# Kernel optimization log

Measured on AMD Instinct MI355X. Metric: run time of the kernel, lower is better.

Reference implementation:

```python
import jax, jax.numpy as jnp
import numpy as np

DIM = 2048
NUM_HEADS = 16
HEAD_DIM = DIM // NUM_HEADS
HIDDEN = 4 * DIM
EPS = 1e-6


def rmsnorm(x, w):
    # Faithful to source: weight * (x * dim**-0.5 / sqrt(mean(x^2) + eps))
    scale = DIM ** -0.5
    norm = jnp.sqrt(jnp.mean(x * x, axis=-1, keepdims=True) + EPS)
    return w * (x * scale / norm)


def setup_inputs() -> dict:
    key = jax.random.key(0)
    ks = jax.random.split(key, 10)
    def init(k, shape, fan_in):
        return jax.random.normal(k, shape, dtype=jnp.float32) * (fan_in ** -0.5)
    return {
        "x": jax.random.normal(ks[0], (2, 2048, DIM), dtype=jnp.float32),
        "norm1_w": jnp.ones((DIM,), dtype=jnp.float32),
        "wq": init(ks[1], (DIM, DIM), DIM),
        "wk": init(ks[2], (HEAD_DIM, DIM), DIM),
        "wv": init(ks[3], (HEAD_DIM, DIM), DIM),
        "wo": init(ks[4], (DIM, DIM), DIM),
        "norm2_w": jnp.ones((DIM,), dtype=jnp.float32),
        "w1": init(ks[5], (HIDDEN, DIM), DIM),
        "w2": init(ks[6], (DIM, HIDDEN), HIDDEN),
        "w3": init(ks[7], (HIDDEN, DIM), DIM),
    }


def reference(x, norm1_w, wq, wk, wv, wo, norm2_w, w1, w2, w3):
    B, S, _ = x.shape
    # --- Multi-Query Attention (pre-norm) ---
    h = rmsnorm(x, norm1_w)
    q = h @ wq.T                                  # [B,S,D]
    k = h @ wk.T                                  # [B,S,hd] (shared across heads)
    v = h @ wv.T                                  # [B,S,hd]
    q = q.reshape(B, S, NUM_HEADS, HEAD_DIM)
    # scores: q @ k^T / sqrt(hd); k is broadcast (repeated) across heads
    scores = jnp.einsum('bshd,btd->bhst', q, k) / (HEAD_DIM ** 0.5)  # [B,H,S,S]
    probs = jax.nn.softmax(scores, axis=-1)
    attn = jnp.einsum('bhst,btd->bshd', probs, v).reshape(B, S, DIM)
    x = x + attn @ wo.T
    # --- SwiGLU FFN (pre-norm) ---
    h = rmsnorm(x, norm2_w)
    ffn = (jax.nn.silu(h @ w1.T) * (h @ w3.T)) @ w2.T
    return x + ffn
```

## Files before the change

kernel.cpp:

```cpp
#include <hip/hip_runtime.h>
#include <hip/hip_bf16.h>

typedef __attribute__((ext_vector_type(4))) float f32x4;
typedef __attribute__((ext_vector_type(8))) short s16x8;
typedef __attribute__((ext_vector_type(4))) short s16x4;
typedef __attribute__((ext_vector_type(2))) short s16x2;

#define MFMA_BF16 __builtin_amdgcn_mfma_f32_16x16x32_bf16

__device__ inline short f2bf(float f) {
  unsigned u = __float_as_uint(f);
  u = (u + 0x7FFFu + ((u >> 16) & 1u)) >> 16;
  return (short)u;
}
__device__ inline float bf2f(short s) {
  return __uint_as_float(((unsigned)(unsigned short)s) << 16);
}

#define DPPF(x, ctrl) __int_as_float(__builtin_amdgcn_update_dpp( \
    __float_as_int(x), __float_as_int(x), ctrl, 0xF, 0xF, false))
__device__ inline float rowmax16(float x) {
  x = fmaxf(x, DPPF(x, 0xB1));
  x = fmaxf(x, DPPF(x, 0x4E));
  x = fmaxf(x, DPPF(x, 0x124));
  x = fmaxf(x, DPPF(x, 0x128));
  return x;
}
__device__ inline float rowsum16(float x) {
  x += DPPF(x, 0xB1);
  x += DPPF(x, 0x4E);
  x += DPPF(x, 0x124);
  x += DPPF(x, 0x128);
  return x;
}

__global__ __launch_bounds__(256) void cvt_kernel(
    const float* __restrict__ in, short* __restrict__ out, int n, float scale)
{
  int idx = (blockIdx.x * 256 + threadIdx.x) * 8;
  if (idx >= n) return;
  f32x4 a = *(const f32x4*)(in + idx);
  f32x4 b = *(const f32x4*)(in + idx + 4);
  s16x8 o;
  #pragma unroll
  for (int j = 0; j < 4; ++j) { o[j] = f2bf(a[j] * scale); o[4 + j] = f2bf(b[j] * scale); }
  *(s16x8*)(out + idx) = o;
}

__global__ __launch_bounds__(256) void rmsnorm_kernel(
    const float* __restrict__ x, const float* __restrict__ w, short* __restrict__ out)
{
  size_t row = blockIdx.x;
  const float* xr = x + row * 2048;
  int base = threadIdx.x * 8;
  f32x4 a = *(const f32x4*)(xr + base);
  f32x4 b = *(const f32x4*)(xr + base + 4);
  float ss = a[0]*a[0] + a[1]*a[1] + a[2]*a[2] + a[3]*a[3]
           + b[0]*b[0] + b[1]*b[1] + b[2]*b[2] + b[3]*b[3];
  #pragma unroll
  for (int off = 1; off < 64; off <<= 1) ss += __shfl_xor(ss, off, 64);
  __shared__ float red[4];
  if ((threadIdx.x & 63) == 0) red[threadIdx.x >> 6] = ss;
  __syncthreads();
  float tot = red[0] + red[1] + red[2] + red[3];
  float rn = rsqrtf(tot * (1.0f / 2048.0f) + 1e-6f) * 0.022097086912079608f;
  f32x4 wa = *(const f32x4*)(w + base);
  f32x4 wb = *(const f32x4*)(w + base + 4);
  s16x8 o;
  #pragma unroll
  for (int j = 0; j < 4; ++j) {
    o[j]     = f2bf(a[j] * wa[j] * rn);
    o[4 + j] = f2bf(b[j] * wb[j] * rn);
  }
  *(s16x8*)(out + row * 2048 + base) = o;
}

template <int MODE>
__global__ __launch_bounds__(256, 2) void gemm_bt_kernel(
    const short* __restrict__ A, const short* __restrict__ B,
    void* __restrict__ Cv, const float* __restrict__ resid,
    int M, int N, int K)
{
  __shared__ short As[128 * 32];
  __shared__ short Bs[128 * 32];
  int tid = threadIdx.x;
  int lane = tid & 63;
  int w = tid >> 6;
  int r = lane & 15, g = lane >> 4;
  int wr = w >> 1, wc = w & 1;
  size_t row0 = (size_t)blockIdx.y * 128;
  size_t col0 = (size_t)blockIdx.x * 128;

  f32x4 acc[4][4];
  #pragma unroll
  for (int i = 0; i < 4; ++i)
    #pragma unroll
    for (int j = 0; j < 4; ++j) acc[i][j] = (f32x4){0.f, 0.f, 0.f, 0.f};

  const short* Ablk = A + row0 * K;
  const short* Bblk = B + col0 * K;
  int arow = tid >> 2;
  int akk = (tid & 3) << 3;

  for (int k0 = 0; k0 < K; k0 += 32) {
    #pragma unroll
    for (int i = 0; i < 2; ++i) {
      int chunk = i * 256 + tid;
      int rr = i * 64 + arow;
      __builtin_amdgcn_global_load_lds(
          (const __attribute__((address_space(1))) unsigned int*)(Ablk + (size_t)rr * K + k0 + akk),
          (__attribute__((address_space(3))) unsigned int*)(&As[chunk * 8]), 16, 0, 0);
      __builtin_amdgcn_global_load_lds(
          (const __attribute__((address_space(1))) unsigned int*)(Bblk + (size_t)rr * K + k0 + akk),
          (__attribute__((address_space(3))) unsigned int*)(&Bs[chunk * 8]), 16, 0, 0);
    }
    __syncthreads();
    s16x8 af[4], bfr[4];
    #pragma unroll
    for (int mm = 0; mm < 4; ++mm)
      af[mm] = *(const s16x8*)(&As[(wr * 64 + mm * 16 + r) * 32 + g * 8]);
    #pragma unroll
    for (int nn = 0; nn < 4; ++nn)
      bfr[nn] = *(const s16x8*)(&Bs[(wc * 64 + nn * 16 + r) * 32 + g * 8]);
    #pragma unroll
    for (int mm = 0; mm < 4; ++mm)
      #pragma unroll
      for (int nn = 0; nn < 4; ++nn)
        acc[mm][nn] = MFMA_BF16(af[mm], bfr[nn], acc[mm][nn], 0, 0, 0);
    __syncthreads();
  }

  #pragma unroll
  for (int mm = 0; mm < 4; ++mm) {
    #pragma unroll
    for (int nn = 0; nn < 4; ++nn) {
      #pragma unroll
      for (int j = 0; j < 4; ++j) {
        size_t rr = row0 + wr * 64 + mm * 16 + g * 4 + j;
        size_t cc = col0 + wc * 64 + nn * 16 + r;
        size_t idx = rr * (size_t)N + cc;
        if constexpr (MODE == 0) {
          ((short*)Cv)[idx] = f2bf(acc[mm][nn][j]);
        } else if constexpr (MODE == 1) {
          ((float*)Cv)[idx] = acc[mm][nn][j] + resid[idx];
        } else {
          short* gp = (short*)Cv;
          float gv = bf2f(gp[idx]);
          float sg = gv / (1.0f + __expf(-gv));
          gp[idx] = f2bf(sg * acc[mm][nn][j]);
        }
      }
    }
  }
}


#define STAGEA1(T)                                                             \
  _Pragma("unroll")                                                            \
  for (int i = 0; i < 4; ++i) {                                                \
    int lc = i * 256 + tid;                                                    \
    int rw = lc >> 3, ch = lc & 7;                                             \
    __builtin_amdgcn_global_load_lds(                                          \
        (const __attribute__((address_space(1))) unsigned int*)                \
            (Ablk + (size_t)rw * K + (T) * 64 + ((ch ^ (rw & 7)) << 3)),       \
        (__attribute__((address_space(3))) unsigned int*)                      \
            (&As[(T) & 1][lc * 8]), 16, 0, 0);                                 \
  }

#define STAGEB1(T)                                                             \
  _Pragma("unroll")                                                            \
  for (int i = 0; i < 4; ++i) {                                                \
    int lc = i * 256 + tid;                                                    \
    int rw = lc >> 3, ch = lc & 7;                                             \
    __builtin_amdgcn_global_load_lds(                                          \
        (const __attribute__((address_space(1))) unsigned int*)                \
            (Bblk + (size_t)rw * K + (T) * 64 + ((ch ^ (rw & 7)) << 3)),       \
        (__attribute__((address_space(3))) unsigned int*)                      \
            (&Bs[(T) & 1][lc * 8]), 16, 0, 0);                                 \
  }

#define LDK(KS, D)                                                             \
  _Pragma("unroll")                                                            \
  for (int mi = 0; mi < 4; ++mi) {                                             \
    int rowa = wr * 64 + mi * 16 + r;                                          \
    aR[mi] = *(const s16x8*)(&As[D][rowa * 64 + (((KS) * 4 + g) ^ (rowa & 7)) * 8]); \
  }                                                                            \
  _Pragma("unroll")                                                            \
  for (int ni = 0; ni < 4; ++ni) {                                             \
    int rowb = wc * 64 + ni * 16 + r;                                          \
    bR[ni] = *(const s16x8*)(&Bs[D][rowb * 64 + (((KS) * 4 + g) ^ (rowb & 7)) * 8]); \
  }

#define MF16A                                                                  \
  __builtin_amdgcn_s_setprio(1);                                               \
  _Pragma("unroll")                                                            \
  for (int mi = 0; mi < 4; ++mi)                                               \
    _Pragma("unroll")                                                          \
    for (int ni = 0; ni < 4; ++ni)                                             \
      acc[mi][ni] = MFMA_BF16(aR[mi], bR[ni], acc[mi][ni], 0, 0, 0);           \
  __builtin_amdgcn_s_setprio(0);

#define BAR __builtin_amdgcn_s_barrier()

template <int MODE>
__global__ __launch_bounds__(256, 2) void gemm128_kernel(
    const short* __restrict__ A, const short* __restrict__ B,
    void* __restrict__ Cv, const float* __restrict__ resid,
    int M, int N, int K)
{
  __shared__ short As[2][128 * 64];
  __shared__ short Bs[2][128 * 64];

  int tid = threadIdx.x;
  int lane = tid & 63;
  int w = tid >> 6;
  int r = lane & 15, g = lane >> 4;
  int wr = w >> 1, wc = w & 1;

  int nwg = gridDim.x * gridDim.y;
  int orig = blockIdx.y * gridDim.x + blockIdx.x;
  int swz = (orig & 7) * (nwg >> 3) + (orig >> 3);
  int bx = swz % gridDim.x, by = swz / gridDim.x;
  size_t row0 = (size_t)by * 128;
  size_t col0 = (size_t)bx * 128;

  const short* Ablk = A + row0 * K;
  const short* Bblk = B + col0 * K;

  f32x4 acc[4][4];
  #pragma unroll
  for (int i = 0; i < 4; ++i)
    #pragma unroll
    for (int j = 0; j < 4; ++j) acc[i][j] = (f32x4){0.f, 0.f, 0.f, 0.f};

  s16x8 aR[4], bR[4];
  int NT = K >> 6;

  STAGEA1(0); STAGEB1(0);

  for (int t = 0; t < NT; ++t) {
    int d = t & 1;
    bool nl = (t < NT - 1);
    if (nl) {
      STAGEA1(t + 1); STAGEB1(t + 1);
      asm volatile("s_waitcnt vmcnt(8)" ::: "memory");
    } else {
      asm volatile("s_waitcnt vmcnt(0)" ::: "memory");
    }
    BAR;
    LDK(0, d);
    MF16A;
    LDK(1, d);
    MF16A;
    BAR;
  }

  #pragma unroll
  for (int mi = 0; mi < 4; ++mi) {
    #pragma unroll
    for (int ni = 0; ni < 4; ++ni) {
      #pragma unroll
      for (int j = 0; j < 4; ++j) {
        size_t rr = row0 + wr * 64 + mi * 16 + g * 4 + j;
        size_t cc = col0 + wc * 64 + ni * 16 + r;
        size_t idx = rr * (size_t)N + cc;
        if constexpr (MODE == 0) {
          ((short*)Cv)[idx] = f2bf(acc[mi][ni][j]);
        } else if constexpr (MODE == 1) {
          ((float*)Cv)[idx] = acc[mi][ni][j] + resid[idx];
        } else {
          short* gp = (short*)Cv;
          float gv = bf2f(gp[idx]);
          float sg = gv / (1.0f + __expf(-gv));
          gp[idx] = f2bf(sg * acc[mi][ni][j]);
        }
      }
    }
  }
}

__global__ __launch_bounds__(256) void transpose_v_kernel(
    const short* __restrict__ kv, short* __restrict__ vt)
{
  __shared__ short t[64][65];
  int b = blockIdx.z;
  int s0 = blockIdx.x * 64;
  int d0 = blockIdx.y * 64;
  int tid = threadIdx.x;
  #pragma unroll
  for (int i = 0; i < 16; ++i) {
    int e = i * 256 + tid;
    int sr = e >> 6, dc = e & 63;
    t[sr][dc] = kv[(size_t)(b * 2048 + s0 + sr) * 256 + 128 + d0 + dc];
  }
  __syncthreads();
  #pragma unroll
  for (int i = 0; i < 16; ++i) {
    int e = i * 256 + tid;
    int dr = e >> 6, sc = e & 63;
    vt[(size_t)b * 128 * 2048 + (size_t)(d0 + dr) * 2048 + s0 + sc] = t[sc][dr];
  }
}

__global__ __launch_bounds__(256, 2) void attn_kernel(
    const short* __restrict__ q, const short* __restrict__ kv,
    const short* __restrict__ vt, short* __restrict__ out)
{
  const int S = 2048;
  int tid = threadIdx.x;
  int w = tid >> 6;
  int lane = tid & 63;
  int r = lane & 15, g = lane >> 4;
  int h = blockIdx.y, b = blockIdx.z;
  int qrow0 = blockIdx.x * 128 + w * 32;

  __shared__ short Ks[2][4096];
  __shared__ short Vs[2][4096];
  __shared__ short Ps[4][32][40];

  const short* kvsrc = kv + (size_t)b * S * 256;
  const short* vsrc  = vt + (size_t)b * 128 * S;

  const short* qbase = q + ((size_t)(b * S + qrow0 + r)) * 2048 + h * 128;
  s16x8 qa[2][4];
  #pragma unroll
  for (int gq = 0; gq < 2; ++gq)
    #pragma unroll
    for (int dc = 0; dc < 4; ++dc)
      qa[gq][dc] = *(const s16x8*)(qbase + gq * 16 * 2048 + dc * 32 + g * 8);

  f32x4 o[2][8];
  #pragma unroll
  for (int gq = 0; gq < 2; ++gq)
    #pragma unroll
    for (int dt = 0; dt < 8; ++dt) o[gq][dt] = (f32x4){0.f, 0.f, 0.f, 0.f};
  float m[2][4], l[2][4];
  #pragma unroll
  for (int gq = 0; gq < 2; ++gq)
    #pragma unroll
    for (int j = 0; j < 4; ++j) { m[gq][j] = -1e30f; l[gq][j] = 0.f; }

#define STAGE(KVT, BSEL)                                                        \
  {                                                                             \
    int kv0s = (KVT) * 32;                                                      \
    _Pragma("unroll")                                                           \
    for (int i = 0; i < 2; ++i) {                                               \
      int c = w * 64 + lane + i * 256;                                          \
      int krow = c >> 4, kcp = c & 15;                                          \
      __builtin_amdgcn_global_load_lds(                                         \
          (const __attribute__((address_space(1))) unsigned int*)               \
              (kvsrc + (size_t)(kv0s + krow) * 256 + ((kcp ^ (krow & 7)) << 3)),\
          (__attribute__((address_space(3))) unsigned int*)(&Ks[BSEL][c * 8]),  \
          16, 0, 0);                                                            \
      int vrow = c >> 2, vcp = c & 3;                                           \
      __builtin_amdgcn_global_load_lds(                                         \
          (const __attribute__((address_space(1))) unsigned int*)               \
              (vsrc + (size_t)vrow * S + kv0s + ((vcp ^ (vrow & 3)) << 3)),     \
          (__attribute__((address_space(3))) unsigned int*)(&Vs[BSEL][c * 8]),  \
          16, 0, 0);                                                            \
    }                                                                           \
  }

  STAGE(0, 0);
  __syncthreads();

  for (int it = 0; it < 64; ++it) {
    int cur = it & 1;
    if (it < 63) STAGE(it + 1, cur ^ 1);

    s16x8 kc0[4], kc1[4], vb[8];
    #pragma unroll
    for (int dc = 0; dc < 4; ++dc) {
      kc0[dc] = *(const s16x8*)(&Ks[cur][r * 128 + (((dc * 4 + g) ^ (r & 7)) << 3)]);
      kc1[dc] = *(const s16x8*)(&Ks[cur][(16 + r) * 128 + (((dc * 4 + g) ^ (r & 7)) << 3)]);
    }
    #pragma unroll
    for (int dt = 0; dt < 8; ++dt)
      vb[dt] = *(const s16x8*)(&Vs[cur][(dt * 16 + r) * 32 + ((g ^ (r & 3)) << 3)]);

    f32x4 sc0[2], sc1[2];
    #pragma unroll
    for (int gq = 0; gq < 2; ++gq) { sc0[gq] = (f32x4){0.f,0.f,0.f,0.f}; sc1[gq] = (f32x4){0.f,0.f,0.f,0.f}; }
    __builtin_amdgcn_s_setprio(1);
    #pragma unroll
    for (int dc = 0; dc < 4; ++dc) {
      #pragma unroll
      for (int gq = 0; gq < 2; ++gq) {
        sc0[gq] = MFMA_BF16(qa[gq][dc], kc0[dc], sc0[gq], 0, 0, 0);
        sc1[gq] = MFMA_BF16(qa[gq][dc], kc1[dc], sc1[gq], 0, 0, 0);
      }
    }
    __builtin_amdgcn_s_setprio(0);

    float p0[2][4], p1[2][4];
    #pragma unroll
    for (int gq = 0; gq < 2; ++gq) {
      float mx[4];
      #pragma unroll
      for (int j = 0; j < 4; ++j) mx[j] = rowmax16(fmaxf(sc0[gq][j], sc1[gq][j]));
      bool nd = (mx[0] > m[gq][0] + 8.f) | (mx[1] > m[gq][1] + 8.f)
              | (mx[2] > m[gq][2] + 8.f) | (mx[3] > m[gq][3] + 8.f);
      if (__any(nd)) {
        #pragma unroll
        for (int j = 0; j < 4; ++j) {
          float mn = fmaxf(m[gq][j], mx[j]);
          float alpha = __expf(m[gq][j] - mn);
          m[gq][j] = mn;
          l[gq][j] *= alpha;
          #pragma unroll
          for (int dt = 0; dt < 8; ++dt) o[gq][dt][j] *= alpha;
        }
      }
      #pragma unroll
      for (int j = 0; j < 4; ++j) {
        p0[gq][j] = __expf(sc0[gq][j] - m[gq][j]);
        p1[gq][j] = __expf(sc1[gq][j] - m[gq][j]);
        l[gq][j] += p0[gq][j] + p1[gq][j];
      }
      #pragma unroll
      for (int j = 0; j < 4; ++j) {
        Ps[w][gq * 16 + g * 4 + j][r]      = f2bf(p0[gq][j]);
        Ps[w][gq * 16 + g * 4 + j][16 + r] = f2bf(p1[gq][j]);
      }
    }
    asm volatile("s_waitcnt lgkmcnt(0)" ::: "memory");
    __builtin_amdgcn_sched_barrier(0);
    s16x8 pa0 = *(const s16x8*)(&Ps[w][r][g * 8]);
    s16x8 pa1 = *(const s16x8*)(&Ps[w][16 + r][g * 8]);
    __builtin_amdgcn_s_setprio(1);
    #pragma unroll
    for (int dt = 0; dt < 8; ++dt) {
      o[0][dt] = MFMA_BF16(pa0, vb[dt], o[0][dt], 0, 0, 0);
      o[1][dt] = MFMA_BF16(pa1, vb[dt], o[1][dt], 0, 0, 0);
    }
    __builtin_amdgcn_s_setprio(0);
    __syncthreads();
  }

  #pragma unroll
  for (int gq = 0; gq < 2; ++gq) {
    float linv[4];
    #pragma unroll
    for (int j = 0; j < 4; ++j) linv[j] = 1.0f / rowsum16(l[gq][j]);
    short* ob = out + ((size_t)(b * S + qrow0 + gq * 16)) * 2048 + h * 128;
    #pragma unroll
    for (int dt = 0; dt < 8; ++dt)
      #pragma unroll
      for (int j = 0; j < 4; ++j)
        ob[(size_t)(g * 4 + j) * 2048 + dt * 16 + r] = f2bf(o[gq][dt][j] * linv[j]);
  }
#undef STAGE
}

extern "C" void kernel_launch(void* const* d_in, const int* in_sizes, int n_in,
                              void* d_out, int out_size, void* d_ws, size_t ws_size,
                              hipStream_t stream) {
  const float* x   = (const float*)d_in[0];
  const float* n1w = (const float*)d_in[1];
  const float* wq  = (const float*)d_in[2];
  const float* wk  = (const float*)d_in[3];
  const float* wv  = (const float*)d_in[4];
  const float* wo  = (const float*)d_in[5];
  const float* n2w = (const float*)d_in[6];
  const float* w1  = (const float*)d_in[7];
  const float* w2  = (const float*)d_in[8];
  const float* w3  = (const float*)d_in[9];
  float* out = (float*)d_out;
  char* ws = (char*)d_ws;
  const size_t MB = 1ull << 20;
  short* wqb  = (short*)(ws);
  short* wob  = (short*)(ws + 8 * MB);
  short* w1b  = (short*)(ws + 16 * MB);
  short* w2b  = (short*)(ws + 48 * MB);
  short* w3b  = (short*)(ws + 80 * MB);
  short* wkvb = (short*)(ws + 112 * MB);
  short* h1   = (short*)(ws + 113 * MB);
  short* gbuf = (short*)(ws + 129 * MB);
  short* qb   = (short*)(ws + 129 * MB);
  short* kvb  = (short*)(ws + 145 * MB);
  short* vtb  = (short*)(ws + 147 * MB);

  const float qscale = 0.08838834764831845f;
  cvt_kernel<<<2048, 256, 0, stream>>>(wq, wqb, 4194304, qscale);
  cvt_kernel<<<128,  256, 0, stream>>>(wk, wkvb, 262144, 1.0f);
  cvt_kernel<<<128,  256, 0, stream>>>(wv, wkvb + 262144, 262144, 1.0f);
  cvt_kernel<<<2048, 256, 0, stream>>>(wo, wob, 4194304, 1.0f);
  cvt_kernel<<<8192, 256, 0, stream>>>(w1, w1b, 16777216, 1.0f);
  cvt_kernel<<<8192, 256, 0, stream>>>(w2, w2b, 16777216, 1.0f);
  cvt_kernel<<<8192, 256, 0, stream>>>(w3, w3b, 16777216, 1.0f);

  rmsnorm_kernel<<<4096, 256, 0, stream>>>(x, n1w, h1);
  gemm128_kernel<0><<<dim3(16, 32), 256, 0, stream>>>(h1, wqb, qb, nullptr, 4096, 2048, 2048);
  gemm_bt_kernel<0><<<dim3(2, 32), 256, 0, stream>>>(h1, wkvb, kvb, nullptr, 4096, 256, 2048);
  transpose_v_kernel<<<dim3(32, 2, 2), 256, 0, stream>>>(kvb, vtb);
  attn_kernel<<<dim3(16, 16, 2), 256, 0, stream>>>(qb, kvb, vtb, h1);
  gemm128_kernel<1><<<dim3(16, 32), 256, 0, stream>>>(h1, wob, out, x, 4096, 2048, 2048);
  rmsnorm_kernel<<<4096, 256, 0, stream>>>(out, n2w, h1);
  gemm128_kernel<0><<<dim3(64, 32), 256, 0, stream>>>(h1, w1b, gbuf, nullptr, 4096, 8192, 2048);
  gemm128_kernel<2><<<dim3(64, 32), 256, 0, stream>>>(h1, w3b, gbuf, nullptr, 4096, 8192, 2048);
  gemm128_kernel<1><<<dim3(16, 32), 256, 0, stream>>>(gbuf, w2b, out, out, 4096, 2048, 8192);
}
```

Measured before the change: 890.7 us.

## Fuse w1 and w3 GEMMs into one dual-accumulator kernel with SiLU epilogue

Replaces the two separate FFN up-projection GEMMs (w1, then w3 with a read-modify-write SiLU gating epilogue) with a single kernel. It loads each A tile once, multiplies it against both weight tiles into two accumulator sets, and writes silu(acc1)*acc3 directly. This removes a second pass over the activations, the bf16 write and re-read of the intermediate gate buffer, and one launch. In exchange it doubles accumulator registers (launch bounds 256,2) and uses a shorter K-tile of 32 with a new LDS swizzle, which may lower occupancy or MFMA efficiency.

Result: faster. 829.8 us (-6.8%).

```diff
diff --git a/kernel.cpp b/kernel.cpp
--- a/kernel.cpp
+++ b/kernel.cpp
@@ -141,19 +141,13 @@
         size_t idx = rr * (size_t)N + cc;
         if constexpr (MODE == 0) {
           ((short*)Cv)[idx] = f2bf(acc[mm][nn][j]);
-        } else if constexpr (MODE == 1) {
+        } else {
           ((float*)Cv)[idx] = acc[mm][nn][j] + resid[idx];
-        } else {
-          short* gp = (short*)Cv;
-          float gv = bf2f(gp[idx]);
-          float sg = gv / (1.0f + __expf(-gv));
-          gp[idx] = f2bf(sg * acc[mm][nn][j]);
         }
       }
     }
   }
 }
-
 
 #define STAGEA1(T)                                                             \
   _Pragma("unroll")                                                            \
@@ -266,14 +260,111 @@
         size_t idx = rr * (size_t)N + cc;
         if constexpr (MODE == 0) {
           ((short*)Cv)[idx] = f2bf(acc[mi][ni][j]);
-        } else if constexpr (MODE == 1) {
+        } else {
           ((float*)Cv)[idx] = acc[mi][ni][j] + resid[idx];
-        } else {
-          short* gp = (short*)Cv;
-          float gv = bf2f(gp[idx]);
-          float sg = gv / (1.0f + __expf(-gv));
-          gp[idx] = f2bf(sg * acc[mi][ni][j]);
         }
+      }
+    }
+  }
+}
+
+
+#define STG13(T, BASE, DST)                                                    \
+  _Pragma("unroll")                                                            \
+  for (int i = 0; i < 2; ++i) {                                                \
+    int lc = i * 256 + tid;                                                    \
+    int rw = lc >> 2, ch = lc & 3;                                             \
+    __builtin_amdgcn_global_load_lds(                                          \
+        (const __attribute__((address_space(1))) unsigned int*)                \
+            (BASE + (size_t)rw * K + (T) * 32 + ((ch ^ ((rw >> 1) & 3)) << 3)),\
+        (__attribute__((address_space(3))) unsigned int*)                      \
+            (&DST[(T) & 1][lc * 8]), 16, 0, 0);                                \
+  }
+
+__global__ __launch_bounds__(256, 2) void gemm_w13_kernel(
+    const short* __restrict__ A, const short* __restrict__ B1,
+    const short* __restrict__ B3, short* __restrict__ C,
+    int M, int N, int K)
+{
+  __shared__ short As[2][128 * 32];
+  __shared__ short B1s[2][128 * 32];
+  __shared__ short B3s[2][128 * 32];
+
+  int tid = threadIdx.x;
+  int lane = tid & 63;
+  int w = tid >> 6;
+  int r = lane & 15, g = lane >> 4;
+  int wr = w >> 1, wc = w & 1;
+
+  int nwg = gridDim.x * gridDim.y;
+  int orig = blockIdx.y * gridDim.x + blockIdx.x;
+  int swz = (orig & 7) * (nwg >> 3) + (orig >> 3);
+  int bx = swz % gridDim.x, by = swz / gridDim.x;
+  size_t row0 = (size_t)by * 128;
+  size_t col0 = (size_t)bx * 128;
+
+  const short* Ablk  = A  + row0 * K;
+  const short* B1blk = B1 + col0 * K;
+  const short* B3blk = B3 + col0 * K;
+
+  f32x4 acc1[4][4], acc3[4][4];
+  #pragma unroll
+  for (int i = 0; i < 4; ++i)
+    #pragma unroll
+    for (int j = 0; j < 4; ++j) {
+      acc1[i][j] = (f32x4){0.f, 0.f, 0.f, 0.f};
+      acc3[i][j] = (f32x4){0.f, 0.f, 0.f, 0.f};
+    }
+
+  s16x8 aR[4], b1R[4], b3R[4];
+  int NT = K >> 5;
+
+  STG13(0, Ablk, As); STG13(0, B1blk, B1s); STG13(0, B3blk, B3s);
+
+  for (int t = 0; t < NT; ++t) {
+    int d = t & 1;
+    bool nl = (t < NT - 1);
+    if (nl) {
+      STG13(t + 1, Ablk, As); STG13(t + 1, B1blk, B1s); STG13(t + 1, B3blk, B3s);
+      asm volatile("s_waitcnt vmcnt(6)" ::: "memory");
+    } else {
+      asm volatile("s_waitcnt vmcnt(0)" ::: "memory");
+    }
+    BAR;
+    #pragma unroll
+    for (int mi = 0; mi < 4; ++mi) {
+      int rowa = wr * 64 + mi * 16 + r;
+      aR[mi] = *(const s16x8*)(&As[d][rowa * 32 + ((g ^ ((rowa >> 1) & 3)) << 3)]);
+    }
+    #pragma unroll
+    for (int ni = 0; ni < 4; ++ni) {
+      int rowb = wc * 64 + ni * 16 + r;
+      b1R[ni] = *(const s16x8*)(&B1s[d][rowb * 32 + ((g ^ ((rowb >> 1) & 3)) << 3)]);
+      b3R[ni] = *(const s16x8*)(&B3s[d][rowb * 32 + ((g ^ ((rowb >> 1) & 3)) << 3)]);
+    }
+    __builtin_amdgcn_s_setprio(1);
+    #pragma unroll
+    for (int mi = 0; mi < 4; ++mi)
+      #pragma unroll
+      for (int ni = 0; ni < 4; ++ni) {
+        acc1[mi][ni] = MFMA_BF16(aR[mi], b1R[ni], acc1[mi][ni], 0, 0, 0);
+        acc3[mi][ni] = MFMA_BF16(aR[mi], b3R[ni], acc3[mi][ni], 0, 0, 0);
+      }
+    __builtin_amdgcn_s_setprio(0);
+    BAR;
+  }
+
+  #pragma unroll
+  for (int mi = 0; mi < 4; ++mi) {
+    #pragma unroll
+    for (int ni = 0; ni < 4; ++ni) {
+      #pragma unroll
+      for (int j = 0; j < 4; ++j) {
+        size_t rr = row0 + wr * 64 + mi * 16 + g * 4 + j;
+        size_t cc = col0 + wc * 64 + ni * 16 + r;
+        float gv = acc1[mi][ni][j];
+        float sg = gv / (1.0f + __expf(-gv));
+        C[rr * (size_t)N + cc] = f2bf(sg * acc3[mi][ni][j]);
       }
     }
   }
@@ -496,7 +587,6 @@
   attn_kernel<<<dim3(16, 16, 2), 256, 0, stream>>>(qb, kvb, vtb, h1);
   gemm128_kernel<1><<<dim3(16, 32), 256, 0, stream>>>(h1, wob, out, x, 4096, 2048, 2048);
   rmsnorm_kernel<<<4096, 256, 0, stream>>>(out, n2w, h1);
-  gemm128_kernel<0><<<dim3(64, 32), 256, 0, stream>>>(h1, w1b, gbuf, nullptr, 4096, 8192, 2048);
-  gemm128_kernel<2><<<dim3(64, 32), 256, 0, stream>>>(h1, w3b, gbuf, nullptr, 4096, 8192, 2048);
+  gemm_w13_kernel<<<dim3(64, 32), 256, 0, stream>>>(h1, w1b, w3b, gbuf, 4096, 8192, 2048);
   gemm128_kernel<1><<<dim3(16, 32), 256, 0, stream>>>(gbuf, w2b, out, out, 4096, 2048, 8192);
 }
```
